# Kernel tuning notes

Hardware: AMD Instinct MI355X
Metric: run time of the kernel (lower is better)

Reference implementation:

```python
import jax, jax.numpy as jnp
import numpy as np

C = 128
N = 4096
B = 4
NEG = -9e15


def _bn(x, g, b):
    # training-mode BatchNorm1d over (batch, N); x: [B, C, N]
    mean = x.mean(axis=(0, 2), keepdims=True)
    var = x.var(axis=(0, 2), keepdims=True)  # biased, like torch BN
    xh = (x - mean) * jax.lax.rsqrt(var + 1e-5)
    return xh * g[None, :, None] + b[None, :, None]


def _sa(x, mask2, wqk, wv, bv, wt, bt, g, b):
    # x: [B, C, N]; wqk: [C//4, C] (q and k share weights)
    xq = jnp.einsum('oc,bcn->bno', wqk, x)          # [B, N, C/4]
    xk = jnp.einsum('oc,bcm->bom', wqk, x)          # [B, C/4, N]
    energy = jnp.einsum('bno,bom->bnm', xq, xk)     # [B, N, N]
    energy = jnp.where(mask2, energy, NEG)
    attn = jax.nn.softmax(energy, axis=-1)
    # offset-attention: column-wise L1 renormalization
    attn = attn / (1e-9 + attn.sum(axis=1, keepdims=True))
    xv = jnp.einsum('oc,bcn->bon', wv, x) + bv[None, :, None]
    x_r = jnp.einsum('bcn,bnm->bcm', xv, attn)      # [B, C, N]
    x_r = jax.nn.relu(_bn(jnp.einsum('oc,bcn->bon', wt, x - x_r) + bt[None, :, None], g, b))
    return x + x_r


def setup_inputs() -> dict:
    key = jax.random.key(0)
    ks = jax.random.split(key, 12)
    s = 1.0 / np.sqrt(C)
    return {
        'x': jax.random.normal(ks[0], (B, C, N), jnp.float32),
        'mask': jax.random.randint(ks[1], (B, N), 0, 2, jnp.int32),
        'w1': jax.random.normal(ks[2], (C, C), jnp.float32) * s,
        'g1': jnp.ones((C,), jnp.float32),
        'b1': jnp.zeros((C,), jnp.float32),
        'w2': jax.random.normal(ks[3], (C, C), jnp.float32) * s,
        'g2': jnp.ones((C,), jnp.float32),
        'b2': jnp.zeros((C,), jnp.float32),
        'wqk': jax.random.normal(ks[4], (4, C // 4, C), jnp.float32) * s,
        'wv': jax.random.normal(ks[5], (4, C, C), jnp.float32) * s,
        'bv': jax.random.normal(ks[6], (4, C), jnp.float32) * 0.01,
        'wt': jax.random.normal(ks[7], (4, C, C), jnp.float32) * s,
        'bt': jax.random.normal(ks[8], (4, C), jnp.float32) * 0.01,
        'sg': jnp.ones((4, C), jnp.float32),
        'sb': jnp.zeros((4, C), jnp.float32),
    }


def reference(x, mask, w1, g1, b1, w2, g2, b2, wqk, wv, bv, wt, bt, sg, sb):
    m = mask.astype(bool)
    mask2 = m[:, :, None] & m[:, None, :]           # [B, N, N]
    x = jax.nn.relu(_bn(jnp.einsum('oc,bcn->bon', w1, x), g1, b1))
    x = jax.nn.relu(_bn(jnp.einsum('oc,bcn->bon', w2, x), g2, b2))
    outs = []
    h = x
    for i in range(4):
        h = _sa(h, mask2, wqk[i], wv[i], bv[i], wt[i], bt[i], sg[i], sb[i])
        outs.append(h)
    return jnp.concatenate(outs, axis=1)            # [B, 4C, N]
```

## Files before the change

### kernel.cpp

```cpp
#include <hip/hip_runtime.h>
#include <hip/hip_fp16.h>

constexpr int C = 128;
constexpr int N = 4096;
constexpr int B = 4;

typedef _Float16 f16x8 __attribute__((ext_vector_type(8)));
typedef _Float16 f16x4 __attribute__((ext_vector_type(4)));
typedef float    f32x4 __attribute__((ext_vector_type(4)));

__global__ __launch_bounds__(256) void k_wcvt(const float* __restrict__ w1,
                                              const float* __restrict__ w2,
                                              const float* __restrict__ wv,
                                              const float* __restrict__ wt,
                                              const float* __restrict__ wqk,
                                              _Float16* __restrict__ WF) {
  const int g = blockIdx.x * 256 + threadIdx.x;
  const float* src; int off;
  if (g < 4096)       { src = w1;  off = g; }
  else if (g < 8192)  { src = w2;  off = g - 4096; }
  else if (g < 24576) { src = wv;  off = g - 8192; }
  else if (g < 40960) { src = wt;  off = g - 24576; }
  else                { src = wqk; off = g - 40960; }
  const float4 v = ((const float4*)src)[off];
  f16x4 h = {(_Float16)v.x, (_Float16)v.y, (_Float16)v.z, (_Float16)v.w};
  *(f16x4*)&WF[(size_t)g * 4] = h;
}

__global__ __launch_bounds__(1024) void k_mask(const int* __restrict__ mask,
                                               int* __restrict__ psum,
                                               int* __restrict__ nvb) {
  const int b = blockIdx.x, tid = threadIdx.x;
  __shared__ int wsum[16];
  const int4 mv = *(const int4*)&mask[b * N + tid * 4];
  const int m0 = (mv.x != 0), m1 = (mv.y != 0), m2 = (mv.z != 0), m3 = (mv.w != 0);
  const int s0 = m0, s1 = s0 + m1, s2 = s1 + m2, s3 = s2 + m3;
  const int lane = tid & 63, w = tid >> 6;
  int sc = s3;
#pragma unroll
  for (int o = 1; o < 64; o <<= 1) {
    const int v = __shfl_up(sc, o, 64);
    if (lane >= o) sc += v;
  }
  if (lane == 63) wsum[w] = sc;
  __syncthreads();
  if (tid < 16) {
    int v = wsum[tid];
#pragma unroll
    for (int o = 1; o < 16; o <<= 1) {
      const int u = __shfl_up(v, o, 64);
      if (tid >= o) v += u;
    }
    wsum[tid] = v;
  }
  __syncthreads();
  const int excl = ((w > 0) ? wsum[w - 1] : 0) + sc - s3;
  int4 pv;
  pv.x = excl; pv.y = excl + s0; pv.z = excl + s1; pv.w = excl + s2;
  *(int4*)&psum[b * N + tid * 4] = pv;
  if (tid == 0) nvb[b] = wsum[15];
}

template<bool BIAS, bool STAT, bool F16IN>
__global__ __launch_bounds__(512) void k_gwm(const _Float16* __restrict__ WF,
                                             const void* __restrict__ Xv,
                                             const float* __restrict__ bias,
                                             _Float16* __restrict__ Y,
                                             float* __restrict__ bnpart) {
  __shared__ _Float16 XT[64 * 136];
  __shared__ float statP[4][64], statQ[4][64];
  const int tid = threadIdx.x;
  const int n0 = blockIdx.x * 64, oh = blockIdx.y, b = blockIdx.z;
  if constexpr (F16IN) {
    const _Float16* Xb = (const _Float16*)Xv + (size_t)(b * C) * N + n0;
#pragma unroll
    for (int i = 0; i < 2; i++) {
      const int idx = tid + i * 512;
      const int c = idx >> 3, q = idx & 7;
      const f16x8 v = *(const f16x8*)&Xb[(size_t)c * N + q * 8];
#pragma unroll
      for (int e = 0; e < 8; e++) XT[(q * 8 + e) * 136 + c] = v[e];
    }
  } else {
    const float* Xb = (const float*)Xv + (size_t)(b * C) * N + n0;
#pragma unroll
    for (int i = 0; i < 4; i++) {
      const int idx = tid + i * 512;
      const int c = idx >> 4, q = idx & 15;
      const float4 v = *(const float4*)&Xb[(size_t)c * N + q * 4];
      XT[(q * 4 + 0) * 136 + c] = (_Float16)v.x;
      XT[(q * 4 + 1) * 136 + c] = (_Float16)v.y;
      XT[(q * 4 + 2) * 136 + c] = (_Float16)v.z;
      XT[(q * 4 + 3) * 136 + c] = (_Float16)v.w;
    }
  }
  __syncthreads();
  const int w = tid >> 6, lane = tid & 63, quad = lane >> 4, lr = lane & 15;
  const int nt = w & 3, og = w >> 2;
  const int ob[2] = {oh * 64 + og * 16, oh * 64 + (og + 2) * 16};
  f16x8 aW[2][4];
#pragma unroll
  for (int t = 0; t < 2; t++)
#pragma unroll
    for (int kc = 0; kc < 4; kc++)
      aW[t][kc] = *(const f16x8*)&WF[(size_t)(ob[t] + lr) * 128 + kc * 32 + quad * 8];
  f32x4 acc[2];
  acc[0] = (f32x4){0.f, 0.f, 0.f, 0.f};
  acc[1] = (f32x4){0.f, 0.f, 0.f, 0.f};
#pragma unroll
  for (int kc = 0; kc < 4; kc++) {
    const f16x8 bf = *(const f16x8*)&XT[(nt * 16 + lr) * 136 + kc * 32 + quad * 8];
    acc[0] = __builtin_amdgcn_mfma_f32_16x16x32_f16(aW[0][kc], bf, acc[0], 0, 0, 0);
    acc[1] = __builtin_amdgcn_mfma_f32_16x16x32_f16(aW[1][kc], bf, acc[1], 0, 0, 0);
  }
#pragma unroll
  for (int t = 0; t < 2; t++) {
#pragma unroll
    for (int r = 0; r < 4; r++) {
      const int o = ob[t] + quad * 4 + r;
      const float val = acc[t][r] + (BIAS ? bias[o] : 0.f);
      Y[(size_t)(b * C + o) * N + n0 + nt * 16 + lr] = (_Float16)val;
      if (STAT) {
        float s = val, q = val * val;
        s += __shfl_xor(s, 1, 64); q += __shfl_xor(q, 1, 64);
        s += __shfl_xor(s, 2, 64); q += __shfl_xor(q, 2, 64);
        s += __shfl_xor(s, 4, 64); q += __shfl_xor(q, 4, 64);
        s += __shfl_xor(s, 8, 64); q += __shfl_xor(q, 8, 64);
        if (lr == 0) { statP[nt][o - oh * 64] = s; statQ[nt][o - oh * 64] = q; }
      }
    }
  }
  if (STAT) {
    __syncthreads();
    if (tid < 64) {
      const int o = oh * 64 + tid;
      const float s = statP[0][tid] + statP[1][tid] + statP[2][tid] + statP[3][tid];
      const float q = statQ[0][tid] + statQ[1][tid] + statQ[2][tid] + statQ[3][tid];
      const int part = blockIdx.x * 4 + b;
      bnpart[o * 1024 + part] = s;
      bnpart[o * 1024 + 512 + part] = q;
    }
  }
}

__global__ __launch_bounds__(256) void k_qv(const _Float16* __restrict__ WFv,
                                            const _Float16* __restrict__ WFqk,
                                            const float* __restrict__ X,
                                            const float* __restrict__ bv,
                                            const int* __restrict__ mask,
                                            const int* __restrict__ psum,
                                            _Float16* __restrict__ XVc,
                                            _Float16* __restrict__ QT,
                                            _Float16* __restrict__ QTc,
                                            float* __restrict__ xvp) {
  __shared__ _Float16 XT[32 * 136];
  __shared__ float SP[2][128];
  const int tid = threadIdx.x;
  const int n0 = blockIdx.x * 32, b = blockIdx.y;
  const float* Xb = X + (size_t)(b * C) * N + n0;
#pragma unroll
  for (int i = 0; i < 4; i++) {
    const int idx = tid + i * 256;
    const int c = idx >> 3, q = idx & 7;
    const float4 v = *(const float4*)&Xb[(size_t)c * N + q * 4];
    XT[(q * 4 + 0) * 136 + c] = (_Float16)v.x;
    XT[(q * 4 + 1) * 136 + c] = (_Float16)v.y;
    XT[(q * 4 + 2) * 136 + c] = (_Float16)v.z;
    XT[(q * 4 + 3) * 136 + c] = (_Float16)v.w;
  }
  __syncthreads();
  const int w = tid >> 6, lane = tid & 63, quad = lane >> 4, lr = lane & 15;
  const int nt = w & 1, og = w >> 1;
  const int n = n0 + nt * 16 + lr;
  const int vld = mask[b * N + n] != 0;
  const int jc = psum[b * N + n];
  f32x4 acc[5];
  const _Float16* Aptr[5];
  int otl[5];
#pragma unroll
  for (int j = 0; j < 5; j++) {
    acc[j] = (f32x4){0.f, 0.f, 0.f, 0.f};
    const int ot = og + 2 * j;
    otl[j] = ot;
    Aptr[j] = (ot < 8) ? (WFv + (size_t)(ot * 16 + lr) * 128)
                       : (WFqk + (size_t)((ot - 8) * 16 + lr) * 128);
  }
#pragma unroll
  for (int kc = 0; kc < 4; kc++) {
    const f16x8 bf = *(const f16x8*)&XT[(nt * 16 + lr) * 136 + kc * 32 + quad * 8];
#pragma unroll
    for (int j = 0; j < 5; j++) {
      const f16x8 a = *(const f16x8*)&Aptr[j][kc * 32 + quad * 8];
      acc[j] = __builtin_amdgcn_mfma_f32_16x16x32_f16(a, bf, acc[j], 0, 0, 0);
    }
  }
#pragma unroll
  for (int j = 0; j < 5; j++) {
    const int ot = otl[j];
    if (ot < 8) {
      float v[4];
#pragma unroll
      for (int r = 0; r < 4; r++) v[r] = acc[j][r] + bv[ot * 16 + quad * 4 + r];
      if (vld) {
#pragma unroll
        for (int r = 0; r < 4; r++)
          XVc[(size_t)(b * C + ot * 16 + quad * 4 + r) * N + jc] = (_Float16)v[r];
      }
      float s[4];
#pragma unroll
      for (int r = 0; r < 4; r++) s[r] = vld ? 0.f : v[r];
#pragma unroll
      for (int o = 1; o <= 8; o <<= 1) {
#pragma unroll
        for (int r = 0; r < 4; r++) s[r] += __shfl_xor(s[r], o, 64);
      }
      if (lr == 0) {
#pragma unroll
        for (int r = 0; r < 4; r++) SP[nt][ot * 16 + quad * 4 + r] = s[r];
      }
    } else {
      f16x4 qv;
#pragma unroll
      for (int r = 0; r < 4; r++) qv[r] = (_Float16)acc[j][r];
      const int qo = (ot - 8) * 16 + quad * 4;
      *(f16x4*)&QT[((size_t)b * N + n) * 32 + qo] = qv;
      if (vld) *(f16x4*)&QTc[((size_t)b * N + jc) * 32 + qo] = qv;
    }
  }
  __syncthreads();
  if (tid < 128)
    xvp[(size_t)(b * C + tid) * 128 + blockIdx.x] = SP[0][tid] + SP[1][tid];
}

__global__ __launch_bounds__(512) void k_sm(const _Float16* __restrict__ QTc,
                                            const int* __restrict__ nvb,
                                            const float* __restrict__ xvp,
                                            float* __restrict__ xvi,
                                            float2* __restrict__ rowst) {
  const int b = blockIdx.y, tid = threadIdx.x;
  if (blockIdx.x == 256) {
    __shared__ float xr[128][4];
    const int c = tid >> 2, q = tid & 3;
    const float* src = xvp + (size_t)(b * C + c) * 128 + q * 32;
    float v = 0.f;
#pragma unroll
    for (int i = 0; i < 32; i++) v += src[i];
    xr[c][q] = v;
    __syncthreads();
    if (tid < 128) xvi[b * C + tid] = xr[tid][0] + xr[tid][1] + xr[tid][2] + xr[tid][3];
    return;
  }
  const int Nv = nvb[b];
  const int NvpB = (Nv + 63) & ~63;
  const int n0 = blockIdx.x * 16;
  if (n0 >= NvpB) return;
  __shared__ float redM[8][16], redS[8][16];
  const _Float16* Qb = QTc + (size_t)b * N * 32;
  const int w = tid >> 6, lane = tid & 63, quad = lane >> 4, lr = lane & 15;
  const f16x8 aF = *(const f16x8*)&Qb[(size_t)(n0 + lr) * 32 + quad * 8];
  float mx[4] = {-3e38f, -3e38f, -3e38f, -3e38f};
  float s[4] = {0.f, 0.f, 0.f, 0.f};
  for (int ms = 0; ms < NvpB; ms += 128) {
    const int mrow = ms + w * 16 + lr;
    const f16x8 bF = *(const f16x8*)&Qb[(size_t)mrow * 32 + quad * 8];
    f32x4 d = (f32x4){0.f, 0.f, 0.f, 0.f};
    d = __builtin_amdgcn_mfma_f32_16x16x32_f16(aF, bF, d, 0, 0, 0);
    const float bias = (mrow < Nv) ? 0.0f : -1e30f;
#pragma unroll
    for (int r = 0; r < 4; r++) {
      const float dv = d[r] + bias;
      if (dv > mx[r]) {
        s[r] *= __expf(mx[r] - dv);
        mx[r] = dv;
      }
      s[r] += __expf(dv - mx[r]);
    }
  }
#pragma unroll
  for (int r = 0; r < 4; r++) {
#pragma unroll
    for (int o = 1; o <= 8; o <<= 1) {
      const float mo = __shfl_xor(mx[r], o, 64);
      const float so = __shfl_xor(s[r], o, 64);
      const float mn = fmaxf(mx[r], mo);
      s[r] = s[r] * __expf(mx[r] - mn) + so * __expf(mo - mn);
      mx[r] = mn;
    }
  }
  if (lr == 0)
#pragma unroll
    for (int r = 0; r < 4; r++) {
      redM[w][quad * 4 + r] = mx[r];
      redS[w][quad * 4 + r] = s[r];
    }
  __syncthreads();
  if (tid < 16) {
    float M = redM[0][tid];
#pragma unroll
    for (int k = 1; k < 8; k++) M = fmaxf(M, redM[k][tid]);
    float tot = 0.f;
#pragma unroll
    for (int k = 0; k < 8; k++) tot += redS[k][tid] * __expf(redM[k][tid] - M);
    const int row = n0 + tid;
    const bool valid = row < Nv;
    float2 rv;
    rv.x = valid ? M : 1e30f;
    rv.y = valid ? (1.0f / tot) : 0.0f;
    rowst[b * N + row] = rv;
  }
}

__global__ __launch_bounds__(512, 4) void k_pv(const _Float16* __restrict__ QT,
                                               const _Float16* __restrict__ QTc,
                                               const _Float16* __restrict__ XVc,
                                               const _Float16* __restrict__ WFt,
                                               const float* __restrict__ H,
                                               const int* __restrict__ mask,
                                               const float2* __restrict__ rowst,
                                               const int* __restrict__ nvb,
                                               const float* __restrict__ xvi,
                                               const float* __restrict__ bt,
                                               _Float16* __restrict__ T2h,
                                               float* __restrict__ bnpart) {
  __shared__ _Float16 XVs[2][128 * 72];
  __shared__ _Float16 PsT[2][32 * 72];
  __shared__ float colPart[4][32];
  __shared__ float colS[32];
  const int tid = threadIdx.x;
  const int m0 = blockIdx.x * 32, b = blockIdx.y;
  const int Nv = nvb[b];
  const int ns = ((Nv + 63) & ~63) >> 6;
  const _Float16* Qa = QT + (size_t)b * N * 32;
  const _Float16* Qc = QTc + (size_t)b * N * 32;
  const _Float16* XVb = XVc + (size_t)(b * C) * N;
  const float2* rsB = rowst + (size_t)b * N;
  const int w = tid >> 6, lane = tid & 63, quad = lane >> 4, lr = lane & 15;
  const int msub = w & 1, nsub = w >> 1;
  const f16x8 bGm = *(const f16x8*)&Qa[(size_t)(m0 + msub * 16 + lr) * 32 + quad * 8];
  const float vmb =
      (mask[b * N + m0 + msub * 16 + lr] != 0) ? 0.0f : -1e30f;
  const int sc0 = tid >> 3, sh0 = tid & 7;
  const int sc1 = sc0 + 64;
  f32x4 acc[2];
  acc[0] = (f32x4){0.f, 0.f, 0.f, 0.f};
  acc[1] = (f32x4){0.f, 0.f, 0.f, 0.f};
  float cs = 0.f;

  auto produce = [&](int k0, int bf) {
    const f16x8 aGn = *(const f16x8*)&Qc[(size_t)(k0 + nsub * 16 + lr) * 32 + quad * 8];
    const f16x8 xv0 = *(const f16x8*)&XVb[(size_t)sc0 * N + k0 + sh0 * 8];
    const f16x8 xv1 = *(const f16x8*)&XVb[(size_t)sc1 * N + k0 + sh0 * 8];
    const int nb = k0 + nsub * 16 + quad * 4;
    const float4 r01 = *(const float4*)&rsB[nb];
    const float4 r23 = *(const float4*)&rsB[nb + 2];
    f32x4 e = (f32x4){0.f, 0.f, 0.f, 0.f};
    e = __builtin_amdgcn_mfma_f32_16x16x32_f16(aGn, bGm, e, 0, 0, 0);
    *(f16x8*)&XVs[bf][sc0 * 72 + sh0 * 8] = xv0;
    *(f16x8*)&XVs[bf][sc1 * 72 + sh0 * 8] = xv1;
    const float p0 = __expf(e[0] - r01.x + vmb) * r01.y;
    const float p1 = __expf(e[1] - r01.z + vmb) * r01.w;
    const float p2 = __expf(e[2] - r23.x + vmb) * r23.y;
    const float p3 = __expf(e[3] - r23.z + vmb) * r23.w;
    cs += (p0 + p1) + (p2 + p3);
    f16x4 pp = {(_Float16)p0, (_Float16)p1, (_Float16)p2, (_Float16)p3};
    *(f16x4*)&PsT[bf][(msub * 16 + lr) * 72 + nsub * 16 + quad * 4] = pp;
  };
  auto consume = [&](int bf) {
    const int c0 = w * 16;
    const f16x8 a0 = *(const f16x8*)&XVs[bf][(c0 + lr) * 72 + quad * 8];
    const f16x8 a1 = *(const f16x8*)&XVs[bf][(c0 + lr) * 72 + 32 + quad * 8];
    const f16x8 b00 = *(const f16x8*)&PsT[bf][lr * 72 + quad * 8];
    const f16x8 b01 = *(const f16x8*)&PsT[bf][lr * 72 + 32 + quad * 8];
    const f16x8 b10 = *(const f16x8*)&PsT[bf][(16 + lr) * 72 + quad * 8];
    const f16x8 b11 = *(const f16x8*)&PsT[bf][(16 + lr) * 72 + 32 + quad * 8];
    acc[0] = __builtin_amdgcn_mfma_f32_16x16x32_f16(a0, b00, acc[0], 0, 0, 0);
    acc[0] = __builtin_amdgcn_mfma_f32_16x16x32_f16(a1, b01, acc[0], 0, 0, 0);
    acc[1] = __builtin_amdgcn_mfma_f32_16x16x32_f16(a0, b10, acc[1], 0, 0, 0);
    acc[1] = __builtin_amdgcn_mfma_f32_16x16x32_f16(a1, b11, acc[1], 0, 0, 0);
  };

  if (ns > 0) produce(0, 0);
  __syncthreads();
  for (int it = 0; it < ns; it += 2) {
    if (it + 1 < ns) produce((it + 1) * 64, 1);
    consume(0);
    __syncthreads();
    if (it + 1 < ns) {
      if (it + 2 < ns) produce((it + 2) * 64, 0);
      consume(1);
      __syncthreads();
    }
  }
  cs += __shfl_xor(cs, 16, 64);
  cs += __shfl_xor(cs, 32, 64);
  if (quad == 0) colPart[nsub][msub * 16 + lr] = cs;
  __syncthreads();
  if (tid < 32)
    colS[tid] = colPart[0][tid] + colPart[1][tid] + colPart[2][tid] + colPart[3][tid];
  __syncthreads();
  const float ninvq = (float)(N - Nv) * 0.000244140625f;
  const float rdiv0 = 1.0f / (1e-9f + colS[lr] + ninvq);
  const float rdiv1 = 1.0f / (1e-9f + colS[16 + lr] + ninvq);
  const int cg = w * 16 + quad * 4;
  _Float16* TdS = &XVs[0][0];
  {
    f16x4 t0, t1;
#pragma unroll
    for (int r = 0; r < 4; r++) {
      const float xadd = xvi[b * C + cg + r] * 0.000244140625f;
      const size_t gi0 = (size_t)(b * C + cg + r) * N + m0 + lr;
      const size_t gi1 = gi0 + 16;
      t0[r] = (_Float16)(H[gi0] - (acc[0][r] + xadd) * rdiv0);
      t1[r] = (_Float16)(H[gi1] - (acc[1][r] + xadd) * rdiv1);
    }
    *(f16x4*)&TdS[lr * 136 + cg] = t0;
    *(f16x4*)&TdS[(16 + lr) * 136 + cg] = t1;
  }
  __syncthreads();
  f32x4 acc2[2];
  acc2[0] = (f32x4){0.f, 0.f, 0.f, 0.f};
  acc2[1] = (f32x4){0.f, 0.f, 0.f, 0.f};
#pragma unroll
  for (int kc = 0; kc < 4; kc++) {
    const f16x8 aT = *(const f16x8*)&WFt[(size_t)(w * 16 + lr) * 128 + kc * 32 + quad * 8];
    const f16x8 bT0 = *(const f16x8*)&TdS[lr * 136 + kc * 32 + quad * 8];
    const f16x8 bT1 = *(const f16x8*)&TdS[(16 + lr) * 136 + kc * 32 + quad * 8];
    acc2[0] = __builtin_amdgcn_mfma_f32_16x16x32_f16(aT, bT0, acc2[0], 0, 0, 0);
    acc2[1] = __builtin_amdgcn_mfma_f32_16x16x32_f16(aT, bT1, acc2[1], 0, 0, 0);
  }
  const int oo = w * 16 + quad * 4;
  const int part = b * 128 + blockIdx.x;
#pragma unroll
  for (int r = 0; r < 4; r++) {
    const float v0 = acc2[0][r] + bt[oo + r];
    const float v1 = acc2[1][r] + bt[oo + r];
    const size_t go = (size_t)(b * C + oo + r) * N + m0 + lr;
    T2h[go] = (_Float16)v0;
    T2h[go + 16] = (_Float16)v1;
    float s = v0 + v1, q = v0 * v0 + v1 * v1;
    s += __shfl_xor(s, 1, 64); q += __shfl_xor(q, 1, 64);
    s += __shfl_xor(s, 2, 64); q += __shfl_xor(q, 2, 64);
    s += __shfl_xor(s, 4, 64); q += __shfl_xor(q, 4, 64);
    s += __shfl_xor(s, 8, 64); q += __shfl_xor(q, 8, 64);
    if (lr == 0) {
      bnpart[(oo + r) * 1024 + part] = s;
      bnpart[(oo + r) * 1024 + 512 + part] = q;
    }
  }
}

template<bool RES, int PARTS>
__global__ __launch_bounds__(256) void k_apply(const _Float16* __restrict__ T2,
                                               const float* __restrict__ bnpart,
                                               const float* __restrict__ gamma,
                                               const float* __restrict__ beta,
                                               float* __restrict__ H,
                                               float* __restrict__ Out) {
  __shared__ float rs[4], rq[4], bc[2];
  const int tid = threadIdx.x;
  const int f = (blockIdx.x * 256 + tid) * 4;
  const int c = (blockIdx.x >> 2) & 127;
  float s, q;
  if (PARTS == 512) {
    s = bnpart[c * 1024 + tid] + bnpart[c * 1024 + 256 + tid];
    q = bnpart[c * 1024 + 512 + tid] + bnpart[c * 1024 + 768 + tid];
  } else {
    s = bnpart[c * 1024 + tid];
    q = bnpart[c * 1024 + 512 + tid];
  }
#pragma unroll
  for (int o = 1; o <= 32; o <<= 1) { s += __shfl_xor(s, o, 64); q += __shfl_xor(q, o, 64); }
  if ((tid & 63) == 0) { rs[tid >> 6] = s; rq[tid >> 6] = q; }
  __syncthreads();
  if (tid == 0) {
    const float st = rs[0] + rs[1] + rs[2] + rs[3];
    const float qt = rq[0] + rq[1] + rq[2] + rq[3];
    const float inv = 1.0f / (B * N);
    const float mean = st * inv;
    const float var = qt * inv - mean * mean;
    const float sc = gamma[c] * rsqrtf(var + 1e-5f);
    bc[0] = sc;
    bc[1] = beta[c] - mean * sc;
  }
  __syncthreads();
  const float sc = bc[0], sh = bc[1];
  const f16x4 t = *(const f16x4*)&T2[f];
  float4 r;
  r.x = fmaxf((float)t[0] * sc + sh, 0.f);
  r.y = fmaxf((float)t[1] * sc + sh, 0.f);
  r.z = fmaxf((float)t[2] * sc + sh, 0.f);
  r.w = fmaxf((float)t[3] * sc + sh, 0.f);
  if (RES) {
    const float4 h = *(const float4*)&H[f];
    r.x += h.x; r.y += h.y; r.z += h.z; r.w += h.w;
    *(float4*)&H[f] = r;
    const int b = f >> 19;
    const int rem = f & (C * N - 1);
    *(float4*)&Out[(size_t)b * (4 * C * N) + rem] = r;
  } else {
    *(float4*)&H[f] = r;
  }
}

extern "C" void kernel_launch(void* const* d_in, const int* in_sizes, int n_in,
                              void* d_out, int out_size, void* d_ws, size_t ws_size,
                              hipStream_t stream) {
  const float* x    = (const float*)d_in[0];
  const int*   mask = (const int*)  d_in[1];
  const float* w1   = (const float*)d_in[2];
  const float* g1   = (const float*)d_in[3];
  const float* b1   = (const float*)d_in[4];
  const float* w2   = (const float*)d_in[5];
  const float* g2   = (const float*)d_in[6];
  const float* b2   = (const float*)d_in[7];
  const float* wqk  = (const float*)d_in[8];
  const float* wv   = (const float*)d_in[9];
  const float* bv   = (const float*)d_in[10];
  const float* wt   = (const float*)d_in[11];
  const float* bt   = (const float*)d_in[12];
  const float* sg   = (const float*)d_in[13];
  const float* sb   = (const float*)d_in[14];
  float* out = (float*)d_out;

  char* p = (char*)d_ws;
  auto alloc = [&](size_t bytes) { char* r = p; p += (bytes + 255) & ~(size_t)255; return r; };
  float*    H      = (float*)   alloc((size_t)B * C * N * 4);
  _Float16* T2h    = (_Float16*)alloc((size_t)B * C * N * 2);
  _Float16* QT     = (_Float16*)alloc((size_t)B * N * 32 * 2);
  _Float16* QTc    = (_Float16*)alloc((size_t)B * N * 32 * 2);
  _Float16* XVc    = (_Float16*)alloc((size_t)B * C * N * 2);
  float2*   rowst  = (float2*)  alloc((size_t)B * N * 8);
  float*    bnpart = (float*)   alloc((size_t)C * 1024 * 4);
  int*      psum   = (int*)     alloc((size_t)B * N * 4);
  int*      nvb    = (int*)     alloc(256);
  float*    xvp    = (float*)   alloc((size_t)B * C * 128 * 4);
  float*    xvi    = (float*)   alloc((size_t)B * C * 4);
  _Float16* WF     = (_Float16*)alloc((size_t)180224 * 2);
  (void)ws_size;
  _Float16* wf1  = WF;
  _Float16* wf2  = WF + 16384;
  _Float16* wfv  = WF + 32768;
  _Float16* wft  = WF + 98304;
  _Float16* wfqk = WF + 163840;

  k_wcvt<<<176, 256, 0, stream>>>(w1, w2, wv, wt, wqk, WF);
  k_mask<<<B, 1024, 0, stream>>>(mask, psum, nvb);
  hipMemsetAsync(QTc, 0, (size_t)B * N * 32 * 2 + (size_t)B * C * N * 2, stream);

  k_gwm<false, true, false><<<dim3(64, 2, B), 512, 0, stream>>>(wf1, x, nullptr, T2h, bnpart);
  k_apply<false, 256><<<2048, 256, 0, stream>>>(T2h, bnpart, g1, b1, H, nullptr);
  k_gwm<false, true, false><<<dim3(64, 2, B), 512, 0, stream>>>(wf2, H, nullptr, T2h, bnpart);
  k_apply<false, 256><<<2048, 256, 0, stream>>>(T2h, bnpart, g2, b2, H, nullptr);

  for (int L = 0; L < 4; L++) {
    k_qv<<<dim3(128, B), 256, 0, stream>>>(wfv + (size_t)L * 16384, wfqk + (size_t)L * 4096,
                                           H, bv + L * C, mask, psum, XVc, QT, QTc, xvp);
    k_sm<<<dim3(257, B), 512, 0, stream>>>(QTc, nvb, xvp, xvi, rowst);
    k_pv<<<dim3(128, B), 512, 0, stream>>>(QT, QTc, XVc, wft + (size_t)L * 16384, H, mask,
                                           rowst, nvb, xvi, bt + L * C, T2h, bnpart);
    k_apply<true, 512><<<2048, 256, 0, stream>>>(T2h, bnpart, sg + L * C, sb + L * C, H,
                                                 out + (size_t)L * C * N);
  }
}
```

Baseline: 412.6 us.

## Halve k_pv block size, double per-wave work, and split loads from compute for overlap

k_pv now runs with 256 threads (4 waves) instead of 512. Each wave computes two 16-row energy tiles and two output-channel tiles, so it holds four accumulators instead of two. The produce step is split into a global-load phase (loadS) issued before consume and a compute/store phase (finS) after it. This lets the next tile's global loads overlap the current MFMA work, at the cost of more registers per thread and fewer waves per block. Grid size is unchanged, so occupancy now depends on LDS use and register pressure.

```diff
diff --git a/kernel.cpp b/kernel.cpp
--- a/kernel.cpp
+++ b/kernel.cpp
@@ -310,7 +310,7 @@
   }
 }
 
-__global__ __launch_bounds__(512, 4) void k_pv(const _Float16* __restrict__ QT,
+__global__ __launch_bounds__(256, 2) void k_pv(const _Float16* __restrict__ QT,
                                                const _Float16* __restrict__ QTc,
                                                const _Float16* __restrict__ XVc,
                                                const _Float16* __restrict__ WFt,
@@ -324,7 +324,7 @@
                                                float* __restrict__ bnpart) {
   __shared__ _Float16 XVs[2][128 * 72];
   __shared__ _Float16 PsT[2][32 * 72];
-  __shared__ float colPart[4][32];
+  __shared__ float colPart[2][32];
   __shared__ float colS[32];
   const int tid = threadIdx.x;
   const int m0 = blockIdx.x * 32, b = blockIdx.y;
@@ -335,116 +335,162 @@
   const _Float16* XVb = XVc + (size_t)(b * C) * N;
   const float2* rsB = rowst + (size_t)b * N;
   const int w = tid >> 6, lane = tid & 63, quad = lane >> 4, lr = lane & 15;
-  const int msub = w & 1, nsub = w >> 1;
+  const int msub = w & 1, nh2 = (w >> 1) * 2;
   const f16x8 bGm = *(const f16x8*)&Qa[(size_t)(m0 + msub * 16 + lr) * 32 + quad * 8];
   const float vmb =
       (mask[b * N + m0 + msub * 16 + lr] != 0) ? 0.0f : -1e30f;
-  const int sc0 = tid >> 3, sh0 = tid & 7;
-  const int sc1 = sc0 + 64;
-  f32x4 acc[2];
-  acc[0] = (f32x4){0.f, 0.f, 0.f, 0.f};
-  acc[1] = (f32x4){0.f, 0.f, 0.f, 0.f};
+  const int s0 = tid >> 3, sh0 = tid & 7;
+  f32x4 acc00 = (f32x4){0.f, 0.f, 0.f, 0.f};
+  f32x4 acc01 = (f32x4){0.f, 0.f, 0.f, 0.f};
+  f32x4 acc10 = (f32x4){0.f, 0.f, 0.f, 0.f};
+  f32x4 acc11 = (f32x4){0.f, 0.f, 0.f, 0.f};
   float cs = 0.f;
-
-  auto produce = [&](int k0, int bf) {
-    const f16x8 aGn = *(const f16x8*)&Qc[(size_t)(k0 + nsub * 16 + lr) * 32 + quad * 8];
-    const f16x8 xv0 = *(const f16x8*)&XVb[(size_t)sc0 * N + k0 + sh0 * 8];
-    const f16x8 xv1 = *(const f16x8*)&XVb[(size_t)sc1 * N + k0 + sh0 * 8];
-    const int nb = k0 + nsub * 16 + quad * 4;
-    const float4 r01 = *(const float4*)&rsB[nb];
-    const float4 r23 = *(const float4*)&rsB[nb + 2];
-    f32x4 e = (f32x4){0.f, 0.f, 0.f, 0.f};
-    e = __builtin_amdgcn_mfma_f32_16x16x32_f16(aGn, bGm, e, 0, 0, 0);
-    *(f16x8*)&XVs[bf][sc0 * 72 + sh0 * 8] = xv0;
-    *(f16x8*)&XVs[bf][sc1 * 72 + sh0 * 8] = xv1;
-    const float p0 = __expf(e[0] - r01.x + vmb) * r01.y;
-    const float p1 = __expf(e[1] - r01.z + vmb) * r01.w;
-    const float p2 = __expf(e[2] - r23.x + vmb) * r23.y;
-    const float p3 = __expf(e[3] - r23.z + vmb) * r23.w;
-    cs += (p0 + p1) + (p2 + p3);
-    f16x4 pp = {(_Float16)p0, (_Float16)p1, (_Float16)p2, (_Float16)p3};
-    *(f16x4*)&PsT[bf][(msub * 16 + lr) * 72 + nsub * 16 + quad * 4] = pp;
+  f16x8 aGn0, aGn1, xv0, xv1, xv2, xv3;
+  float4 ra0, ra1, rb0, rb1;
+
+  auto loadS = [&](int k0) {
+    aGn0 = *(const f16x8*)&Qc[(size_t)(k0 + nh2 * 16 + lr) * 32 + quad * 8];
+    aGn1 = *(const f16x8*)&Qc[(size_t)(k0 + nh2 * 16 + 16 + lr) * 32 + quad * 8];
+    xv0 = *(const f16x8*)&XVb[(size_t)s0 * N + k0 + sh0 * 8];
+    xv1 = *(const f16x8*)&XVb[(size_t)(s0 + 32) * N + k0 + sh0 * 8];
+    xv2 = *(const f16x8*)&XVb[(size_t)(s0 + 64) * N + k0 + sh0 * 8];
+    xv3 = *(const f16x8*)&XVb[(size_t)(s0 + 96) * N + k0 + sh0 * 8];
+    const int nb = k0 + nh2 * 16 + quad * 4;
+    ra0 = *(const float4*)&rsB[nb];
+    ra1 = *(const float4*)&rsB[nb + 2];
+    rb0 = *(const float4*)&rsB[nb + 16];
+    rb1 = *(const float4*)&rsB[nb + 18];
+  };
+  auto finS = [&](int bf) {
+    f32x4 e0 = (f32x4){0.f, 0.f, 0.f, 0.f};
+    f32x4 e1 = (f32x4){0.f, 0.f, 0.f, 0.f};
+    e0 = __builtin_amdgcn_mfma_f32_16x16x32_f16(aGn0, bGm, e0, 0, 0, 0);
+    e1 = __builtin_amdgcn_mfma_f32_16x16x32_f16(aGn1, bGm, e1, 0, 0, 0);
+    *(f16x8*)&XVs[bf][s0 * 72 + sh0 * 8] = xv0;
+    *(f16x8*)&XVs[bf][(s0 + 32) * 72 + sh0 * 8] = xv1;
+    *(f16x8*)&XVs[bf][(s0 + 64) * 72 + sh0 * 8] = xv2;
+    *(f16x8*)&XVs[bf][(s0 + 96) * 72 + sh0 * 8] = xv3;
+    const float p0 = __expf(e0[0] - ra0.x + vmb) * ra0.y;
+    const float p1 = __expf(e0[1] - ra0.z + vmb) * ra0.w;
+    const float p2 = __expf(e0[2] - ra1.x + vmb) * ra1.y;
+    const float p3 = __expf(e0[3] - ra1.z + vmb) * ra1.w;
+    const float p4 = __expf(e1[0] - rb0.x + vmb) * rb0.y;
+    const float p5 = __expf(e1[1] - rb0.z + vmb) * rb0.w;
+    const float p6 = __expf(e1[2] - rb1.x + vmb) * rb1.y;
+    const float p7 = __expf(e1[3] - rb1.z + vmb) * rb1.w;
+    cs += (p0 + p1) + (p2 + p3) + (p4 + p5) + (p6 + p7);
+    f16x4 pp0 = {(_Float16)p0, (_Float16)p1, (_Float16)p2, (_Float16)p3};
+    f16x4 pp1 = {(_Float16)p4, (_Float16)p5, (_Float16)p6, (_Float16)p7};
+    *(f16x4*)&PsT[bf][(msub * 16 + lr) * 72 + nh2 * 16 + quad * 4] = pp0;
+    *(f16x4*)&PsT[bf][(msub * 16 + lr) * 72 + (nh2 + 1) * 16 + quad * 4] = pp1;
   };
   auto consume = [&](int bf) {
-    const int c0 = w * 16;
-    const f16x8 a0 = *(const f16x8*)&XVs[bf][(c0 + lr) * 72 + quad * 8];
-    const f16x8 a1 = *(const f16x8*)&XVs[bf][(c0 + lr) * 72 + 32 + quad * 8];
+    const int c0 = w * 16, c1 = (w + 4) * 16;
+    const f16x8 a00 = *(const f16x8*)&XVs[bf][(c0 + lr) * 72 + quad * 8];
+    const f16x8 a01 = *(const f16x8*)&XVs[bf][(c0 + lr) * 72 + 32 + quad * 8];
+    const f16x8 a10 = *(const f16x8*)&XVs[bf][(c1 + lr) * 72 + quad * 8];
+    const f16x8 a11 = *(const f16x8*)&XVs[bf][(c1 + lr) * 72 + 32 + quad * 8];
     const f16x8 b00 = *(const f16x8*)&PsT[bf][lr * 72 + quad * 8];
     const f16x8 b01 = *(const f16x8*)&PsT[bf][lr * 72 + 32 + quad * 8];
     const f16x8 b10 = *(const f16x8*)&PsT[bf][(16 + lr) * 72 + quad * 8];
     const f16x8 b11 = *(const f16x8*)&PsT[bf][(16 + lr) * 72 + 32 + quad * 8];
-    acc[0] = __builtin_amdgcn_mfma_f32_16x16x32_f16(a0, b00, acc[0], 0, 0, 0);
-    acc[0] = __builtin_amdgcn_mfma_f32_16x16x32_f16(a1, b01, acc[0], 0, 0, 0);
-    acc[1] = __builtin_amdgcn_mfma_f32_16x16x32_f16(a0, b10, acc[1], 0, 0, 0);
-    acc[1] = __builtin_amdgcn_mfma_f32_16x16x32_f16(a1, b11, acc[1], 0, 0, 0);
+    acc00 = __builtin_amdgcn_mfma_f32_16x16x32_f16(a00, b00, acc00, 0, 0, 0);
+    acc00 = __builtin_amdgcn_mfma_f32_16x16x32_f16(a01, b01, acc00, 0, 0, 0);
+    acc01 = __builtin_amdgcn_mfma_f32_16x16x32_f16(a00, b10, acc01, 0, 0, 0);
+    acc01 = __builtin_amdgcn_mfma_f32_16x16x32_f16(a01, b11, acc01, 0, 0, 0);
+    acc10 = __builtin_amdgcn_mfma_f32_16x16x32_f16(a10, b00, acc10, 0, 0, 0);
+    acc10 = __builtin_amdgcn_mfma_f32_16x16x32_f16(a11, b01, acc10, 0, 0, 0);
+    acc11 = __builtin_amdgcn_mfma_f32_16x16x32_f16(a10, b10, acc11, 0, 0, 0);
+    acc11 = __builtin_amdgcn_mfma_f32_16x16x32_f16(a11, b11, acc11, 0, 0, 0);
   };
 
-  if (ns > 0) produce(0, 0);
+  if (ns > 0) { loadS(0); finS(0); }
   __syncthreads();
   for (int it = 0; it < ns; it += 2) {
-    if (it + 1 < ns) produce((it + 1) * 64, 1);
+    const bool h1 = it + 1 < ns;
+    if (h1) loadS((it + 1) * 64);
     consume(0);
+    if (h1) finS(1);
     __syncthreads();
-    if (it + 1 < ns) {
-      if (it + 2 < ns) produce((it + 2) * 64, 0);
+    if (h1) {
+      const bool h2 = it + 2 < ns;
+      if (h2) loadS((it + 2) * 64);
       consume(1);
+      if (h2) finS(0);
       __syncthreads();
     }
   }
   cs += __shfl_xor(cs, 16, 64);
   cs += __shfl_xor(cs, 32, 64);
-  if (quad == 0) colPart[nsub][msub * 16 + lr] = cs;
-  __syncthreads();
-  if (tid < 32)
-    colS[tid] = colPart[0][tid] + colPart[1][tid] + colPart[2][tid] + colPart[3][tid];
+  if (quad == 0) colPart[w >> 1][msub * 16 + lr] = cs;
+  __syncthreads();
+  if (tid < 32) colS[tid] = colPart[0][tid] + colPart[1][tid];
   __syncthreads();
   const float ninvq = (float)(N - Nv) * 0.000244140625f;
   const float rdiv0 = 1.0f / (1e-9f + colS[lr] + ninvq);
   const float rdiv1 = 1.0f / (1e-9f + colS[16 + lr] + ninvq);
-  const int cg = w * 16 + quad * 4;
   _Float16* TdS = &XVs[0][0];
   {
+    const int cg0 = w * 16 + quad * 4;
     f16x4 t0, t1;
 #pragma unroll
     for (int r = 0; r < 4; r++) {
-      const float xadd = xvi[b * C + cg + r] * 0.000244140625f;
-      const size_t gi0 = (size_t)(b * C + cg + r) * N + m0 + lr;
-      const size_t gi1 = gi0 + 16;
-      t0[r] = (_Float16)(H[gi0] - (acc[0][r] + xadd) * rdiv0);
-      t1[r] = (_Float16)(H[gi1] - (acc[1][r] + xadd) * rdiv1);
-    }
-    *(f16x4*)&TdS[lr * 136 + cg] = t0;
-    *(f16x4*)&TdS[(16 + lr) * 136 + cg] = t1;
-  }
-  __syncthreads();
-  f32x4 acc2[2];
-  acc2[0] = (f32x4){0.f, 0.f, 0.f, 0.f};
-  acc2[1] = (f32x4){0.f, 0.f, 0.f, 0.f};
+      const float xadd = xvi[b * C + cg0 + r] * 0.000244140625f;
+      const size_t gi0 = (size_t)(b * C + cg0 + r) * N + m0 + lr;
+      t0[r] = (_Float16)(H[gi0] - (acc00[r] + xadd) * rdiv0);
+      t1[r] = (_Float16)(H[gi0 + 16] - (acc01[r] + xadd) * rdiv1);
+    }
+    *(f16x4*)&TdS[lr * 136 + cg0] = t0;
+    *(f16x4*)&TdS[(16 + lr) * 136 + cg0] = t1;
+    const int cg1 = (w + 4) * 16 + quad * 4;
+#pragma unroll
+    for (int r = 0; r < 4; r++) {
+      const float xadd = xvi[b * C + cg1 + r] * 0.000244140625f;
+      const size_t gi0 = (size_t)(b * C + cg1 + r) * N + m0 + lr;
+      t0[r] = (_Float16)(H[gi0] - (acc10[r] + xadd) * rdiv0);
+      t1[r] = (_Float16)(H[gi0 + 16] - (acc11[r] + xadd) * rdiv1);
+    }
+    *(f16x4*)&TdS[lr * 136 + cg1] = t0;
+    *(f16x4*)&TdS[(16 + lr) * 136 + cg1] = t1;
+  }
+  __syncthreads();
+  f32x4 q00 = (f32x4){0.f, 0.f, 0.f, 0.f};
+  f32x4 q01 = (f32x4){0.f, 0.f, 0.f, 0.f};
+  f32x4 q10 = (f32x4){0.f, 0.f, 0.f, 0.f};
+  f32x4 q11 = (f32x4){0.f, 0.f, 0.f, 0.f};
 #pragma unroll
   for (int kc = 0; kc < 4; kc++) {
-    const f16x8 aT = *(const f16x8*)&WFt[(size_t)(w * 16 + lr) * 128 + kc * 32 + quad * 8];
     const f16x8 bT0 = *(const f16x8*)&TdS[lr * 136 + kc * 32 + quad * 8];
     const f16x8 bT1 = *(const f16x8*)&TdS[(16 + lr) * 136 + kc * 32 + quad * 8];
-    acc2[0] = __builtin_amdgcn_mfma_f32_16x16x32_f16(aT, bT0, acc2[0], 0, 0, 0);
-    acc2[1] = __builtin_amdgcn_mfma_f32_16x16x32_f16(aT, bT1, acc2[1], 0, 0, 0);
-  }
-  const int oo = w * 16 + quad * 4;
+    const f16x8 aT0 = *(const f16x8*)&WFt[(size_t)(w * 16 + lr) * 128 + kc * 32 + quad * 8];
+    const f16x8 aT1 = *(const f16x8*)&WFt[(size_t)((w + 4) * 16 + lr) * 128 + kc * 32 + quad * 8];
+    q00 = __builtin_amdgcn_mfma_f32_16x16x32_f16(aT0, bT0, q00, 0, 0, 0);
+    q01 = __builtin_amdgcn_mfma_f32_16x16x32_f16(aT0, bT1, q01, 0, 0, 0);
+    q10 = __builtin_amdgcn_mfma_f32_16x16x32_f16(aT1, bT0, q10, 0, 0, 0);
+    q11 = __builtin_amdgcn_mfma_f32_16x16x32_f16(aT1, bT1, q11, 0, 0, 0);
+  }
   const int part = b * 128 + blockIdx.x;
 #pragma unroll
-  for (int r = 0; r < 4; r++) {
-    const float v0 = acc2[0][r] + bt[oo + r];
-    const float v1 = acc2[1][r] + bt[oo + r];
-    const size_t go = (size_t)(b * C + oo + r) * N + m0 + lr;
-    T2h[go] = (_Float16)v0;
-    T2h[go + 16] = (_Float16)v1;
-    float s = v0 + v1, q = v0 * v0 + v1 * v1;
-    s += __shfl_xor(s, 1, 64); q += __shfl_xor(q, 1, 64);
-    s += __shfl_xor(s, 2, 64); q += __shfl_xor(q, 2, 64);
-    s += __shfl_xor(s, 4, 64); q += __shfl_xor(q, 4, 64);
-    s += __shfl_xor(s, 8, 64); q += __shfl_xor(q, 8, 64);
-    if (lr == 0) {
-      bnpart[(oo + r) * 1024 + part] = s;
-      bnpart[(oo + r) * 1024 + 512 + part] = q;
+  for (int ot = 0; ot < 2; ot++) {
+    const int oo = (w + ot * 4) * 16 + quad * 4;
+    const f32x4& qa = ot ? q10 : q00;
+    const f32x4& qb = ot ? q11 : q01;
+#pragma unroll
+    for (int r = 0; r < 4; r++) {
+      const float v0 = qa[r] + bt[oo + r];
+      const float v1 = qb[r] + bt[oo + r];
+      const size_t go = (size_t)(b * C + oo + r) * N + m0 + lr;
+      T2h[go] = (_Float16)v0;
+      T2h[go + 16] = (_Float16)v1;
+      float s = v0 + v1, q = v0 * v0 + v1 * v1;
+      s += __shfl_xor(s, 1, 64); q += __shfl_xor(q, 1, 64);
+      s += __shfl_xor(s, 2, 64); q += __shfl_xor(q, 2, 64);
+      s += __shfl_xor(s, 4, 64); q += __shfl_xor(q, 4, 64);
+      s += __shfl_xor(s, 8, 64); q += __shfl_xor(q, 8, 64);
+      if (lr == 0) {
+        bnpart[(oo + r) * 1024 + part] = s;
+        bnpart[(oo + r) * 1024 + 512 + part] = q;
+      }
     }
   }
 }
@@ -556,7 +602,7 @@
     k_qv<<<dim3(128, B), 256, 0, stream>>>(wfv + (size_t)L * 16384, wfqk + (size_t)L * 4096,
                                            H, bv + L * C, mask, psum, XVc, QT, QTc, xvp);
     k_sm<<<dim3(257, B), 512, 0, stream>>>(QTc, nvb, xvp, xvi, rowst);
-    k_pv<<<dim3(128, B), 512, 0, stream>>>(QT, QTc, XVc, wft + (size_t)L * 16384, H, mask,
+    k_pv<<<dim3(128, B), 256, 0, stream>>>(QT, QTc, XVc, wft + (size_t)L * 16384, H, mask,
                                            rowst, nvb, xvi, bt + L * C, T2h, bnpart);
     k_apply<true, 512><<<2048, 256, 0, stream>>>(T2h, bnpart, sg + L * C, sb + L * C, H,
                                                  out + (size_t)L * C * N);
```

Result: slower. 432.2 us (+4.8%).

## Fuse BatchNorm apply into consumer kernels and reduce stats with atomics

Applied to the files above, without the earlier changes.

Removes most standalone BN-apply kernels. BN normalize+ReLU (and the residual add) is now applied on the fly as the next GEMM kernel (k_gwm, k_qvF) loads its input, and only a final apply runs after the last layer. Per-block partial statistics are no longer written to a large partial buffer and re-reduced. They are atomically accumulated into four shards of per-channel sums that each consumer reduces in a tiny prologue. This cuts several launches and full-tensor round trips. In exchange it adds atomics and a stats-buffer memset, and gives order-dependent float sums.

```diff
diff --git a/kernel.cpp b/kernel.cpp
--- a/kernel.cpp
+++ b/kernel.cpp
@@ -8,6 +8,18 @@
 typedef _Float16 f16x8 __attribute__((ext_vector_type(8)));
 typedef _Float16 f16x4 __attribute__((ext_vector_type(4)));
 typedef float    f32x4 __attribute__((ext_vector_type(4)));
+
+__device__ __forceinline__ float2 bn_coef(const float* __restrict__ st, int c,
+                                          const float* __restrict__ gamma,
+                                          const float* __restrict__ beta) {
+  const float s = st[c] + st[256 + c] + st[512 + c] + st[768 + c];
+  const float q = st[128 + c] + st[384 + c] + st[640 + c] + st[896 + c];
+  const float inv = 1.0f / (B * N);
+  const float mean = s * inv;
+  const float var = q * inv - mean * mean;
+  const float sc = gamma[c] * rsqrtf(var + 1e-5f);
+  return {sc, beta[c] - mean * sc};
+}
 
 __global__ __launch_bounds__(256) void k_wcvt(const float* __restrict__ w1,
                                               const float* __restrict__ w2,
@@ -61,25 +73,35 @@
   if (tid == 0) nvb[b] = wsum[15];
 }
 
-template<bool BIAS, bool STAT, bool F16IN>
+template<bool FUSE_BN>
 __global__ __launch_bounds__(512) void k_gwm(const _Float16* __restrict__ WF,
                                              const void* __restrict__ Xv,
-                                             const float* __restrict__ bias,
+                                             const float* __restrict__ st_in,
+                                             const float* __restrict__ gamma,
+                                             const float* __restrict__ beta,
                                              _Float16* __restrict__ Y,
-                                             float* __restrict__ bnpart) {
+                                             float* __restrict__ st_out) {
   __shared__ _Float16 XT[64 * 136];
   __shared__ float statP[4][64], statQ[4][64];
+  __shared__ float bcS[128][2];
   const int tid = threadIdx.x;
   const int n0 = blockIdx.x * 64, oh = blockIdx.y, b = blockIdx.z;
-  if constexpr (F16IN) {
+  if constexpr (FUSE_BN) {
+    if (tid < 128) {
+      const float2 bc = bn_coef(st_in, tid, gamma, beta);
+      bcS[tid][0] = bc.x; bcS[tid][1] = bc.y;
+    }
+    __syncthreads();
     const _Float16* Xb = (const _Float16*)Xv + (size_t)(b * C) * N + n0;
 #pragma unroll
-    for (int i = 0; i < 2; i++) {
+    for (int i = 0; i < 4; i++) {
       const int idx = tid + i * 512;
-      const int c = idx >> 3, q = idx & 7;
-      const f16x8 v = *(const f16x8*)&Xb[(size_t)c * N + q * 8];
-#pragma unroll
-      for (int e = 0; e < 8; e++) XT[(q * 8 + e) * 136 + c] = v[e];
+      const int c = idx >> 4, q = idx & 15;
+      const f16x4 t = *(const f16x4*)&Xb[(size_t)c * N + q * 4];
+      const float sc = bcS[c][0], sh = bcS[c][1];
+#pragma unroll
+      for (int e = 0; e < 4; e++)
+        XT[(q * 4 + e) * 136 + c] = (_Float16)fmaxf((float)t[e] * sc + sh, 0.f);
     }
   } else {
     const float* Xb = (const float*)Xv + (size_t)(b * C) * N + n0;
@@ -118,55 +140,78 @@
 #pragma unroll
     for (int r = 0; r < 4; r++) {
       const int o = ob[t] + quad * 4 + r;
-      const float val = acc[t][r] + (BIAS ? bias[o] : 0.f);
+      const float val = acc[t][r];
       Y[(size_t)(b * C + o) * N + n0 + nt * 16 + lr] = (_Float16)val;
-      if (STAT) {
-        float s = val, q = val * val;
-        s += __shfl_xor(s, 1, 64); q += __shfl_xor(q, 1, 64);
-        s += __shfl_xor(s, 2, 64); q += __shfl_xor(q, 2, 64);
-        s += __shfl_xor(s, 4, 64); q += __shfl_xor(q, 4, 64);
-        s += __shfl_xor(s, 8, 64); q += __shfl_xor(q, 8, 64);
-        if (lr == 0) { statP[nt][o - oh * 64] = s; statQ[nt][o - oh * 64] = q; }
-      }
-    }
-  }
-  if (STAT) {
-    __syncthreads();
-    if (tid < 64) {
-      const int o = oh * 64 + tid;
-      const float s = statP[0][tid] + statP[1][tid] + statP[2][tid] + statP[3][tid];
-      const float q = statQ[0][tid] + statQ[1][tid] + statQ[2][tid] + statQ[3][tid];
-      const int part = blockIdx.x * 4 + b;
-      bnpart[o * 1024 + part] = s;
-      bnpart[o * 1024 + 512 + part] = q;
-    }
-  }
-}
-
-__global__ __launch_bounds__(256) void k_qv(const _Float16* __restrict__ WFv,
-                                            const _Float16* __restrict__ WFqk,
-                                            const float* __restrict__ X,
-                                            const float* __restrict__ bv,
-                                            const int* __restrict__ mask,
-                                            const int* __restrict__ psum,
-                                            _Float16* __restrict__ XVc,
-                                            _Float16* __restrict__ QT,
-                                            _Float16* __restrict__ QTc,
-                                            float* __restrict__ xvp) {
+      float s = val, q = val * val;
+      s += __shfl_xor(s, 1, 64); q += __shfl_xor(q, 1, 64);
+      s += __shfl_xor(s, 2, 64); q += __shfl_xor(q, 2, 64);
+      s += __shfl_xor(s, 4, 64); q += __shfl_xor(q, 4, 64);
+      s += __shfl_xor(s, 8, 64); q += __shfl_xor(q, 8, 64);
+      if (lr == 0) { statP[nt][o - oh * 64] = s; statQ[nt][o - oh * 64] = q; }
+    }
+  }
+  __syncthreads();
+  if (tid < 64) {
+    const int o = oh * 64 + tid;
+    const float s = statP[0][tid] + statP[1][tid] + statP[2][tid] + statP[3][tid];
+    const float q = statQ[0][tid] + statQ[1][tid] + statQ[2][tid] + statQ[3][tid];
+    float* sh = st_out + (blockIdx.x & 3) * 256;
+    atomicAdd(&sh[o], s);
+    atomicAdd(&sh[128 + o], q);
+  }
+}
+
+template<bool RES>
+__global__ __launch_bounds__(256) void k_qvF(const _Float16* __restrict__ WFv,
+                                             const _Float16* __restrict__ WFqk,
+                                             const _Float16* __restrict__ T2,
+                                             const float* __restrict__ st_in,
+                                             const float* __restrict__ gamma,
+                                             const float* __restrict__ beta,
+                                             float* __restrict__ H,
+                                             float* __restrict__ OutS,
+                                             const float* __restrict__ bv,
+                                             const int* __restrict__ mask,
+                                             const int* __restrict__ psum,
+                                             _Float16* __restrict__ XVc,
+                                             _Float16* __restrict__ QT,
+                                             _Float16* __restrict__ QTc,
+                                             float* __restrict__ xvp) {
   __shared__ _Float16 XT[32 * 136];
   __shared__ float SP[2][128];
+  __shared__ float bcS[128][2];
   const int tid = threadIdx.x;
   const int n0 = blockIdx.x * 32, b = blockIdx.y;
-  const float* Xb = X + (size_t)(b * C) * N + n0;
+  if (tid < 128) {
+    const float2 bc = bn_coef(st_in, tid, gamma, beta);
+    bcS[tid][0] = bc.x; bcS[tid][1] = bc.y;
+  }
+  __syncthreads();
+  const _Float16* Tb = T2 + (size_t)(b * C) * N + n0;
 #pragma unroll
   for (int i = 0; i < 4; i++) {
     const int idx = tid + i * 256;
     const int c = idx >> 3, q = idx & 7;
-    const float4 v = *(const float4*)&Xb[(size_t)c * N + q * 4];
-    XT[(q * 4 + 0) * 136 + c] = (_Float16)v.x;
-    XT[(q * 4 + 1) * 136 + c] = (_Float16)v.y;
-    XT[(q * 4 + 2) * 136 + c] = (_Float16)v.z;
-    XT[(q * 4 + 3) * 136 + c] = (_Float16)v.w;
+    const f16x4 t = *(const f16x4*)&Tb[(size_t)c * N + q * 4];
+    const float sc = bcS[c][0], sh = bcS[c][1];
+    float4 h;
+    h.x = fmaxf((float)t[0] * sc + sh, 0.f);
+    h.y = fmaxf((float)t[1] * sc + sh, 0.f);
+    h.z = fmaxf((float)t[2] * sc + sh, 0.f);
+    h.w = fmaxf((float)t[3] * sc + sh, 0.f);
+    const size_t gi = (size_t)(b * C + c) * N + n0 + q * 4;
+    if constexpr (RES) {
+      const float4 ho = *(const float4*)&H[gi];
+      h.x += ho.x; h.y += ho.y; h.z += ho.z; h.w += ho.w;
+      *(float4*)&H[gi] = h;
+      *(float4*)&OutS[(size_t)b * (4 * C * N) + (size_t)c * N + n0 + q * 4] = h;
+    } else {
+      *(float4*)&H[gi] = h;
+    }
+    XT[(q * 4 + 0) * 136 + c] = (_Float16)h.x;
+    XT[(q * 4 + 1) * 136 + c] = (_Float16)h.y;
+    XT[(q * 4 + 2) * 136 + c] = (_Float16)h.z;
+    XT[(q * 4 + 3) * 136 + c] = (_Float16)h.w;
   }
   __syncthreads();
   const int w = tid >> 6, lane = tid & 63, quad = lane >> 4, lr = lane & 15;
@@ -321,7 +366,7 @@
                                                const float* __restrict__ xvi,
                                                const float* __restrict__ bt,
                                                _Float16* __restrict__ T2h,
-                                               float* __restrict__ bnpart) {
+                                               float* __restrict__ st_out) {
   __shared__ _Float16 XVs[2][128 * 72];
   __shared__ _Float16 PsT[2][32 * 72];
   __shared__ float colPart[4][32];
@@ -429,7 +474,7 @@
     acc2[1] = __builtin_amdgcn_mfma_f32_16x16x32_f16(aT, bT1, acc2[1], 0, 0, 0);
   }
   const int oo = w * 16 + quad * 4;
-  const int part = b * 128 + blockIdx.x;
+  float* shd = st_out + (blockIdx.x & 3) * 256;
 #pragma unroll
   for (int r = 0; r < 4; r++) {
     const float v0 = acc2[0][r] + bt[oo + r];
@@ -443,63 +488,32 @@
     s += __shfl_xor(s, 4, 64); q += __shfl_xor(q, 4, 64);
     s += __shfl_xor(s, 8, 64); q += __shfl_xor(q, 8, 64);
     if (lr == 0) {
-      bnpart[(oo + r) * 1024 + part] = s;
-      bnpart[(oo + r) * 1024 + 512 + part] = q;
-    }
-  }
-}
-
-template<bool RES, int PARTS>
-__global__ __launch_bounds__(256) void k_apply(const _Float16* __restrict__ T2,
-                                               const float* __restrict__ bnpart,
-                                               const float* __restrict__ gamma,
-                                               const float* __restrict__ beta,
-                                               float* __restrict__ H,
-                                               float* __restrict__ Out) {
-  __shared__ float rs[4], rq[4], bc[2];
+      atomicAdd(&shd[oo + r], s);
+      atomicAdd(&shd[128 + oo + r], q);
+    }
+  }
+}
+
+__global__ __launch_bounds__(256) void k_applyF(const _Float16* __restrict__ T2,
+                                                const float* __restrict__ st,
+                                                const float* __restrict__ gamma,
+                                                const float* __restrict__ beta,
+                                                const float* __restrict__ H,
+                                                float* __restrict__ Out) {
   const int tid = threadIdx.x;
   const int f = (blockIdx.x * 256 + tid) * 4;
   const int c = (blockIdx.x >> 2) & 127;
-  float s, q;
-  if (PARTS == 512) {
-    s = bnpart[c * 1024 + tid] + bnpart[c * 1024 + 256 + tid];
-    q = bnpart[c * 1024 + 512 + tid] + bnpart[c * 1024 + 768 + tid];
-  } else {
-    s = bnpart[c * 1024 + tid];
-    q = bnpart[c * 1024 + 512 + tid];
-  }
-#pragma unroll
-  for (int o = 1; o <= 32; o <<= 1) { s += __shfl_xor(s, o, 64); q += __shfl_xor(q, o, 64); }
-  if ((tid & 63) == 0) { rs[tid >> 6] = s; rq[tid >> 6] = q; }
-  __syncthreads();
-  if (tid == 0) {
-    const float st = rs[0] + rs[1] + rs[2] + rs[3];
-    const float qt = rq[0] + rq[1] + rq[2] + rq[3];
-    const float inv = 1.0f / (B * N);
-    const float mean = st * inv;
-    const float var = qt * inv - mean * mean;
-    const float sc = gamma[c] * rsqrtf(var + 1e-5f);
-    bc[0] = sc;
-    bc[1] = beta[c] - mean * sc;
-  }
-  __syncthreads();
-  const float sc = bc[0], sh = bc[1];
+  const float2 bc = bn_coef(st, c, gamma, beta);
   const f16x4 t = *(const f16x4*)&T2[f];
+  const float4 h = *(const float4*)&H[f];
   float4 r;
-  r.x = fmaxf((float)t[0] * sc + sh, 0.f);
-  r.y = fmaxf((float)t[1] * sc + sh, 0.f);
-  r.z = fmaxf((float)t[2] * sc + sh, 0.f);
-  r.w = fmaxf((float)t[3] * sc + sh, 0.f);
-  if (RES) {
-    const float4 h = *(const float4*)&H[f];
-    r.x += h.x; r.y += h.y; r.z += h.z; r.w += h.w;
-    *(float4*)&H[f] = r;
-    const int b = f >> 19;
-    const int rem = f & (C * N - 1);
-    *(float4*)&Out[(size_t)b * (4 * C * N) + rem] = r;
-  } else {
-    *(float4*)&H[f] = r;
-  }
+  r.x = fmaxf((float)t[0] * bc.x + bc.y, 0.f) + h.x;
+  r.y = fmaxf((float)t[1] * bc.x + bc.y, 0.f) + h.y;
+  r.z = fmaxf((float)t[2] * bc.x + bc.y, 0.f) + h.z;
+  r.w = fmaxf((float)t[3] * bc.x + bc.y, 0.f) + h.w;
+  const int b = f >> 19;
+  const int rem = f & (C * N - 1);
+  *(float4*)&Out[(size_t)b * (4 * C * N) + rem] = r;
 }
 
 extern "C" void kernel_launch(void* const* d_in, const int* in_sizes, int n_in,
@@ -525,12 +539,13 @@
   char* p = (char*)d_ws;
   auto alloc = [&](size_t bytes) { char* r = p; p += (bytes + 255) & ~(size_t)255; return r; };
   float*    H      = (float*)   alloc((size_t)B * C * N * 4);
-  _Float16* T2h    = (_Float16*)alloc((size_t)B * C * N * 2);
+  _Float16* T2a    = (_Float16*)alloc((size_t)B * C * N * 2);
+  _Float16* T2b    = (_Float16*)alloc((size_t)B * C * N * 2);
   _Float16* QT     = (_Float16*)alloc((size_t)B * N * 32 * 2);
   _Float16* QTc    = (_Float16*)alloc((size_t)B * N * 32 * 2);
   _Float16* XVc    = (_Float16*)alloc((size_t)B * C * N * 2);
+  float*    bnstat = (float*)   alloc((size_t)6 * 1024 * 4);
   float2*   rowst  = (float2*)  alloc((size_t)B * N * 8);
-  float*    bnpart = (float*)   alloc((size_t)C * 1024 * 4);
   int*      psum   = (int*)     alloc((size_t)B * N * 4);
   int*      nvb    = (int*)     alloc(256);
   float*    xvp    = (float*)   alloc((size_t)B * C * 128 * 4);
@@ -542,23 +557,31 @@
   _Float16* wfv  = WF + 32768;
   _Float16* wft  = WF + 98304;
   _Float16* wfqk = WF + 163840;
+  auto st = [&](int k) { return bnstat + (size_t)k * 1024; };
 
   k_wcvt<<<176, 256, 0, stream>>>(w1, w2, wv, wt, wqk, WF);
   k_mask<<<B, 1024, 0, stream>>>(mask, psum, nvb);
-  hipMemsetAsync(QTc, 0, (size_t)B * N * 32 * 2 + (size_t)B * C * N * 2, stream);
-
-  k_gwm<false, true, false><<<dim3(64, 2, B), 512, 0, stream>>>(wf1, x, nullptr, T2h, bnpart);
-  k_apply<false, 256><<<2048, 256, 0, stream>>>(T2h, bnpart, g1, b1, H, nullptr);
-  k_gwm<false, true, false><<<dim3(64, 2, B), 512, 0, stream>>>(wf2, H, nullptr, T2h, bnpart);
-  k_apply<false, 256><<<2048, 256, 0, stream>>>(T2h, bnpart, g2, b2, H, nullptr);
+  hipMemsetAsync(QTc, 0,
+                 (size_t)B * N * 32 * 2 + (size_t)B * C * N * 2 + (size_t)6 * 1024 * 4,
+                 stream);
+
+  k_gwm<false><<<dim3(64, 2, B), 512, 0, stream>>>(wf1, x, nullptr, nullptr, nullptr,
+                                                   T2a, st(0));
+  k_gwm<true><<<dim3(64, 2, B), 512, 0, stream>>>(wf2, T2a, st(0), g1, b1, T2b, st(1));
 
   for (int L = 0; L < 4; L++) {
-    k_qv<<<dim3(128, B), 256, 0, stream>>>(wfv + (size_t)L * 16384, wfqk + (size_t)L * 4096,
-                                           H, bv + L * C, mask, psum, XVc, QT, QTc, xvp);
+    if (L == 0)
+      k_qvF<false><<<dim3(128, B), 256, 0, stream>>>(
+          wfv, wfqk, T2b, st(1), g2, b2, H, nullptr, bv, mask, psum, XVc, QT, QTc, xvp);
+    else
+      k_qvF<true><<<dim3(128, B), 256, 0, stream>>>(
+          wfv + (size_t)L * 16384, wfqk + (size_t)L * 4096, T2a, st(1 + L),
+          sg + (L - 1) * C, sb + (L - 1) * C, H, out + (size_t)(L - 1) * C * N,
+          bv + L * C, mask, psum, XVc, QT, QTc, xvp);
     k_sm<<<dim3(257, B), 512, 0, stream>>>(QTc, nvb, xvp, xvi, rowst);
     k_pv<<<dim3(128, B), 512, 0, stream>>>(QT, QTc, XVc, wft + (size_t)L * 16384, H, mask,
-                                           rowst, nvb, xvi, bt + L * C, T2h, bnpart);
-    k_apply<true, 512><<<2048, 256, 0, stream>>>(T2h, bnpart, sg + L * C, sb + L * C, H,
-                                                 out + (size_t)L * C * N);
-  }
-}
+                                           rowst, nvb, xvi, bt + L * C, T2a, st(2 + L));
+  }
+  k_applyF<<<2048, 256, 0, stream>>>(T2a, st(5), sg + 3 * C, sb + 3 * C, H,
+                                     out + (size_t)3 * C * N);
+}
```

After: 418.5 us. No clear change (+1.4%).
